# Kernel optimization log

Hardware: AMD Instinct MI355X
Metric: run time of the kernel (lower is better)

Reference implementation:

```python
import jax, jax.numpy as jnp
import numpy as np

BN_EPS = 1e-5
NEG_SLOPE = 0.2


def setup_inputs() -> dict:
    key = jax.random.key(0)
    ks = jax.random.split(key, 3)
    B, C, N, O = 8, 64, 4096, 64
    x = jax.random.normal(ks[0], (B, C, N), dtype=jnp.float32)
    W = jax.random.normal(ks[1], (O, 2 * C), dtype=jnp.float32) * 0.05
    gamma = jnp.ones((O,), dtype=jnp.float32)
    beta = jnp.zeros((O,), dtype=jnp.float32)
    run_mean = jnp.zeros((O,), dtype=jnp.float32)
    run_var = jnp.ones((O,), dtype=jnp.float32)
    return {"x": x, "W": W, "gamma": gamma, "beta": beta,
            "run_mean": run_mean, "run_var": run_var, "k": 20}


def _edgeconv(x, W, gamma, beta, run_mean, run_var, k):
    # x: [B, C, N] -> features [B, N, C]
    xt = jnp.transpose(x, (0, 2, 1))                      # [B, N, C]
    # pairwise_distance = -||xi||^2 + 2 xi.xj - ||xj||^2 (negative sq dist)
    sq = jnp.sum(xt * xt, axis=2, keepdims=True)          # [B, N, 1]
    inner = jnp.einsum('bnc,bmc->bnm', xt, xt)            # [B, N, N]
    pd = 2.0 * inner - sq - jnp.transpose(sq, (0, 2, 1))  # [B, N, N]
    _, idx = jax.lax.top_k(pd, k)                         # [B, N, k] nearest (incl. self)
    # gather neighbor features per batch
    neighbors = jax.vmap(lambda f, i: f[i])(xt, idx)      # [B, N, k, C]
    x_exp = xt[:, :, None, :]                             # [B, N, 1, C]
    edge = jnp.concatenate(
        [jnp.broadcast_to(x_exp, neighbors.shape), neighbors - x_exp], axis=3)  # [B,N,k,2C]
    # 1x1 conv == matmul over channel dim
    y = jnp.einsum('bnkc,oc->bnko', edge, W)              # [B, N, k, O]
    scale = gamma / jnp.sqrt(run_var + BN_EPS)
    y = y * scale + (beta - run_mean * scale)
    y = jnp.where(y >= 0, y, NEG_SLOPE * y)               # LeakyReLU(0.2)
    out = jnp.max(y, axis=2)                              # [B, N, O] max over k
    return jnp.transpose(out, (0, 2, 1))                  # [B, O, N]


def reference(x, W, gamma, beta, run_mean, run_var, k):
    return _edgeconv(x, W, gamma, beta, run_mean, run_var, k)
```

## Files before the change

### kernel.cpp

```cpp
#include <hip/hip_runtime.h>

#define B 8
#define C 64
#define N 4096
#define O 64
#define KNN 20
#define PQ 4
#define BN_EPS 1e-5f
#define NEG_SLOPE 0.2f

typedef _Float16 f16x8 __attribute__((ext_vector_type(8)));
typedef float    f32x4 __attribute__((ext_vector_type(4)));
#define MFMA16(a, b, c) __builtin_amdgcn_mfma_f32_16x16x32_f16(a, b, c, 0, 0, 0)

__device__ __forceinline__ void sorted_insert(float (&d)[KNN], int (&id)[KNN],
                                              float r, int m) {
    bool c[KNN];
    #pragma unroll
    for (int j = 0; j < KNN; ++j) c[j] = d[j] < r;
    #pragma unroll
    for (int j = 0; j < KNN - 1; ++j) {
        d[j]  = __builtin_amdgcn_fmed3f(d[j], d[j + 1], r);
        id[j] = c[j + 1] ? id[j + 1] : (c[j] ? m : id[j]);
    }
    d[KNN - 1]  = c[KNN - 1] ? r : d[KNN - 1];
    id[KNN - 1] = c[KNN - 1] ? m : id[KNN - 1];
}

__global__ __launch_bounds__(256) void k_transpose(const float* __restrict__ x,
                                                   float* __restrict__ Xt,
                                                   float* __restrict__ sq,
                                                   char* __restrict__ AHL) {
    __shared__ float lds[C][65];
    int b    = blockIdx.x >> 6;
    int n0   = (blockIdx.x & 63) << 6;
    int lane = threadIdx.x & 63;
    int w    = threadIdx.x >> 6;
    #pragma unroll
    for (int i = 0; i < 16; ++i) {
        int c = w * 16 + i;
        lds[c][lane] = x[(size_t)b * C * N + (size_t)c * N + n0 + lane];
    }
    __syncthreads();
    #pragma unroll
    for (int i = 0; i < 16; ++i) {
        int nl = w * 16 + i;
        Xt[(size_t)b * N * C + (size_t)(n0 + nl) * C + lane] = lds[lane][nl];
    }
    {
        int n_loc = threadIdx.x >> 2;
        int cg    = threadIdx.x & 3;
        float s = 0.f;
        #pragma unroll
        for (int ii = 0; ii < 16; ++ii) {
            float v = lds[cg * 16 + ii][n_loc];
            s = fmaf(v, v, s);
        }
        s += __shfl_xor(s, 1, 64);
        s += __shfl_xor(s, 2, 64);
        if (cg == 0) sq[b * N + n0 + n_loc] = s;
    }
    int s2  = threadIdx.x & 15;
    int rem = threadIdx.x >> 4;
    int qd  = rem & 3;
    int hh  = (rem >> 2) & 1;
    int tt  = rem >> 3;
    int kb  = hh * 32 + qd * 8;
    for (int i = 0; i < 4; ++i) {
        int rowl = i * 16 + s2;
        f16x8 pk;
        #pragma unroll
        for (int ii = 0; ii < 8; ++ii) {
            float v = lds[kb + ii][rowl];
            _Float16 hv = (_Float16)v;
            if (tt) hv = (_Float16)(v - (float)hv);
            pk[ii] = hv;
        }
        char* dst = AHL + ((size_t)b << 20) + (size_t)((n0 >> 4) + i) * 4096
                  + tt * 2048 + hh * 1024 + qd * 256 + s2 * 16;
        *(f16x8*)dst = pk;
    }
}

__global__ __launch_bounds__(256, 2) void k_ab(const float* __restrict__ Xt,
                                               const float* __restrict__ W,
                                               float* __restrict__ av,
                                               float* __restrict__ bv) {
    int b  = blockIdx.x & 7;
    int n0 = ((blockIdx.x >> 3) & 31) << 7;
    int o  = threadIdx.x & 63;
    int w  = __builtin_amdgcn_readfirstlane((int)(threadIdx.x >> 6));
    float wa[C], wb[C];
    #pragma unroll
    for (int c = 0; c < C; ++c) {
        float w1 = W[o * 2 * C + c];
        float w2 = W[o * 2 * C + C + c];
        wa[c] = w1 - w2;
        wb[c] = w2;
    }
    const float* xb = Xt + (size_t)b * N * C;
    for (int i = 0; i < 32; ++i) {
        int n = n0 + w * 32 + i;
        const float4* xr4 = (const float4*)(xb + (size_t)n * C);
        float aa = 0.f, bb = 0.f;
        #pragma unroll
        for (int c4 = 0; c4 < C / 4; ++c4) {
            float4 xv = xr4[c4];
            aa = fmaf(xv.x, wa[c4 * 4 + 0], aa);
            bb = fmaf(xv.x, wb[c4 * 4 + 0], bb);
            aa = fmaf(xv.y, wa[c4 * 4 + 1], aa);
            bb = fmaf(xv.y, wb[c4 * 4 + 1], bb);
            aa = fmaf(xv.z, wa[c4 * 4 + 2], aa);
            bb = fmaf(xv.z, wb[c4 * 4 + 2], bb);
            aa = fmaf(xv.w, wa[c4 * 4 + 3], aa);
            bb = fmaf(xv.w, wb[c4 * 4 + 3], bb);
        }
        size_t oidx = ((size_t)b * N + n) * O + o;
        av[oidx] = aa;
        bv[oidx] = bb;
    }
}

__global__ __launch_bounds__(64, 2) void k_knn(const char* __restrict__ AHL,
                                               const float* __restrict__ sq,
                                               float* __restrict__ pdg,
                                               int* __restrict__ pig) {
    int bid  = blockIdx.x;
    int qg   = bid >> 4;
    int b    = bid & 7;
    int h    = (bid >> 3) & 1;
    int lane = threadIdx.x & 63;
    int quad = lane >> 4;
    const char*  AHLb = AHL + ((size_t)b << 20);
    const float* sqb  = sq + b * N;
    int cbase0 = h * (N / 2);
    const char* Asrc = AHLb + (size_t)cbase0 * 256;

    const char* qb = AHLb + (size_t)qg * 4096 + lane * 16;
    f16x8 bh0 = *(const f16x8*)(qb);
    f16x8 bh1 = *(const f16x8*)(qb + 1024);
    f16x8 bl0 = *(const f16x8*)(qb + 2048);
    f16x8 bl1 = *(const f16x8*)(qb + 3072);

    float d[KNN]; int id[KNN];
    float pv[PQ]; int pi[PQ]; int pc = 0;
    #pragma unroll
    for (int j = 0; j < PQ; ++j) { pv[j] = 0.f; pi[j] = 0; }

    const char* p0 = Asrc + lane * 16;
    f16x8 na0 = *(const f16x8*)(p0);
    f16x8 na1 = *(const f16x8*)(p0 + 1024);
    f16x8 na2 = *(const f16x8*)(p0 + 2048);
    f16x8 na3 = *(const f16x8*)(p0 + 3072);
    float4 nsq = *(const float4*)(sqb + cbase0 + quad * 4);

    #pragma unroll
    for (int it = 0; it < 5; ++it) {
        f16x8 a0 = na0, a1 = na1, a2 = na2, a3 = na3;
        float4 sqv = nsq;
        {
            const char* p = Asrc + (size_t)(it + 1) * 4096 + lane * 16;
            na0 = *(const f16x8*)(p);
            na1 = *(const f16x8*)(p + 1024);
            na2 = *(const f16x8*)(p + 2048);
            na3 = *(const f16x8*)(p + 3072);
            nsq = *(const float4*)(sqb + cbase0 + (it + 1) * 16 + quad * 4);
        }
        f32x4 acc = {0.f, 0.f, 0.f, 0.f};
        acc = MFMA16(a0, bh0, acc);
        acc = MFMA16(a1, bh1, acc);
        acc = MFMA16(a0, bl0, acc);
        acc = MFMA16(a1, bl1, acc);
        acc = MFMA16(a2, bh0, acc);
        acc = MFMA16(a3, bh1, acc);
        int c0 = cbase0 + it * 16 + quad * 4;
        #pragma unroll
        for (int r = 0; r < 4; ++r) {
            float sc = fmaf(2.f, acc[r],
                            -((r == 0) ? sqv.x : (r == 1) ? sqv.y
                                       : (r == 2) ? sqv.z : sqv.w));
            d[it * 4 + r]  = sc;
            id[it * 4 + r] = c0 + r;
        }
    }
    #pragma unroll
    for (int i = 0; i < KNN - 1; ++i) {
        #pragma unroll
        for (int j = 0; j < KNN - 1 - i; ++j) {
            bool sw = d[j] > d[j + 1];
            float tv = d[j]; int ti = id[j];
            d[j]      = sw ? d[j + 1] : d[j];
            id[j]     = sw ? id[j + 1] : id[j];
            d[j + 1]  = sw ? tv : d[j + 1];
            id[j + 1] = sw ? ti : id[j + 1];
        }
    }
    float thr = d[0];
    thr = fmaxf(thr, __shfl_xor(thr, 16, 64));
    thr = fmaxf(thr, __shfl_xor(thr, 32, 64));

    #pragma unroll 1
    for (int it = 5; it < 128; ++it) {
        f16x8 a0 = na0, a1 = na1, a2 = na2, a3 = na3;
        float4 sqv = nsq;
        if (it + 1 < 128) {
            const char* p = Asrc + (size_t)(it + 1) * 4096 + lane * 16;
            na0 = *(const f16x8*)(p);
            na1 = *(const f16x8*)(p + 1024);
            na2 = *(const f16x8*)(p + 2048);
            na3 = *(const f16x8*)(p + 3072);
            nsq = *(const float4*)(sqb + cbase0 + (it + 1) * 16 + quad * 4);
        }
        f32x4 acc = {0.f, 0.f, 0.f, 0.f};
        acc = MFMA16(a0, bh0, acc);
        acc = MFMA16(a1, bh1, acc);
        acc = MFMA16(a0, bl0, acc);
        acc = MFMA16(a1, bl1, acc);
        acc = MFMA16(a2, bh0, acc);
        acc = MFMA16(a3, bh1, acc);
        int c0 = cbase0 + it * 16 + quad * 4;
        #pragma unroll
        for (int r = 0; r < 4; ++r) {
            float sc = fmaf(2.f, acc[r],
                            -((r == 0) ? sqv.x : (r == 1) ? sqv.y
                                       : (r == 2) ? sqv.z : sqv.w));
            if (sc > thr) {
                #pragma unroll
                for (int j = 0; j < PQ; ++j) {
                    bool sel = (pc == j);
                    pv[j] = sel ? sc : pv[j];
                    pi[j] = sel ? (c0 + r) : pi[j];
                }
                ++pc;
            }
            if (__any(pc == PQ)) {
                #pragma unroll
                for (int j = 0; j < PQ; ++j)
                    if (j < pc && pv[j] > d[0]) sorted_insert(d, id, pv[j], pi[j]);
                pc = 0;
                float t = d[0];
                t = fmaxf(t, __shfl_xor(t, 16, 64));
                t = fmaxf(t, __shfl_xor(t, 32, 64));
                thr = fmaxf(thr, t);
            }
        }
    }
    #pragma unroll
    for (int j = 0; j < PQ; ++j)
        if (j < pc && pv[j] > d[0]) sorted_insert(d, id, pv[j], pi[j]);

    #pragma unroll 1
    for (int step = 0; step < 2; ++step) {
        int off = (step == 0) ? 32 : 16;
        bool active = (step == 0) ? (quad < 2) : (quad == 0);
        for (int j = KNN - 1; j >= 0; --j) {
            float rv = __shfl(d[j], lane + off, 64);
            int   ri = __shfl(id[j], lane + off, 64);
            bool ins = active && (rv > d[0]);
            if (!__any(ins)) break;
            if (ins) sorted_insert(d, id, rv, ri);
        }
    }
    if (lane < 16) {
        size_t rr = (size_t)b * N + qg * 16 + lane;
        float* po = pdg + (rr * 2 + h) * KNN;
        int*   qo = pig + (rr * 2 + h) * KNN;
        #pragma unroll
        for (int j = 0; j < KNN; ++j) { po[j] = d[j]; qo[j] = id[j]; }
    }
}

__global__ __launch_bounds__(128) void k_merge(const float* __restrict__ pdg,
                                               const int* __restrict__ pig,
                                               int* __restrict__ knn) {
    __shared__ float sd[128][41];
    __shared__ int   si[128][41];
    int t = threadIdx.x;
    size_t rr = (size_t)blockIdx.x * 128 + t;
    const float* pr = pdg + rr * (2 * KNN);
    const int*   qr = pig + rr * (2 * KNN);
    #pragma unroll
    for (int j = 0; j < 2 * KNN; ++j) { sd[t][j] = pr[j]; si[t][j] = qr[j]; }
    int i = KNN - 1, j = KNN - 1;
    int* op = knn + rr * KNN;
    for (int o = 0; o < KNN; ++o) {
        bool t0 = (j < 0) || (i >= 0 && sd[t][i] >= sd[t][KNN + j]);
        op[o] = t0 ? si[t][i] : si[t][KNN + j];
        if (t0) --i; else --j;
    }
}

__global__ __launch_bounds__(256) void k_out(const float* __restrict__ av,
                                             const float* __restrict__ bv,
                                             const int* __restrict__ knn,
                                             const float* __restrict__ gamma,
                                             const float* __restrict__ beta,
                                             const float* __restrict__ rmean,
                                             const float* __restrict__ rvar,
                                             float* __restrict__ out) {
    __shared__ float lds[64][65];
    int b    = blockIdx.x & 7;
    int n0   = (blockIdx.x >> 3) << 6;
    int lane = threadIdx.x & 63;
    int w    = __builtin_amdgcn_readfirstlane((int)(threadIdx.x >> 6));
    int o    = lane;
    float scale = gamma[o] * rsqrtf(rvar[o] + BN_EPS);
    float bias  = fmaf(-rmean[o], scale, beta[o]);
    const float* bvb = bv + (size_t)b * N * O;
    for (int i = 0; i < 16; ++i) {
        int n = n0 + w * 16 + i;
        const int* kn = knn + ((size_t)b * N + n) * KNN;
        float mx = -3.4e38f, mn = 3.4e38f;
        #pragma unroll
        for (int j = 0; j < KNN; ++j) {
            float v = bvb[(size_t)kn[j] * O + o];
            mx = fmaxf(mx, v);
            mn = fminf(mn, v);
        }
        float a   = av[((size_t)b * N + n) * O + o];
        float sel = (scale >= 0.f) ? (a + mx) : (a + mn);
        float y   = fmaf(sel, scale, bias);
        y = fmaxf(y, NEG_SLOPE * y);
        lds[o][w * 16 + i] = y;
    }
    __syncthreads();
    int r  = threadIdx.x >> 2;
    int c0 = (threadIdx.x & 3) << 4;
    float* ob = out + (size_t)b * O * N + (size_t)r * N + n0;
    #pragma unroll
    for (int j = 0; j < 16; j += 4) {
        float4 v;
        v.x = lds[r][c0 + j + 0];
        v.y = lds[r][c0 + j + 1];
        v.z = lds[r][c0 + j + 2];
        v.w = lds[r][c0 + j + 3];
        *(float4*)(ob + c0 + j) = v;
    }
}

extern "C" void kernel_launch(void* const* d_in, const int* in_sizes, int n_in,
                              void* d_out, int out_size, void* d_ws, size_t ws_size,
                              hipStream_t stream) {
    const float* x     = (const float*)d_in[0];
    const float* W     = (const float*)d_in[1];
    const float* gamma = (const float*)d_in[2];
    const float* beta  = (const float*)d_in[3];
    const float* rmean = (const float*)d_in[4];
    const float* rvar  = (const float*)d_in[5];
    float* out = (float*)d_out;

    char* wsb = (char*)d_ws;
    float* Xt  = (float*)(wsb);
    float* sqn = (float*)(wsb + 8388608);
    float* av  = (float*)(wsb + 8519680);
    float* bvv = (float*)(wsb + 16908288);
    int*   knn = (int*)  (wsb + 25296896);
    char*  AHL =         (wsb + 27918336);
    float* pdg = (float*)(wsb + 36306944);
    int*   pig = (int*)  (wsb + 41549824);

    k_transpose<<<512, 256, 0, stream>>>(x, Xt, sqn, AHL);
    k_ab<<<256, 256, 0, stream>>>(Xt, W, av, bvv);
    k_knn<<<4096, 64, 0, stream>>>(AHL, sqn, pdg, pig);
    k_merge<<<256, 128, 0, stream>>>(pdg, pig, knn);
    k_out<<<512, 256, 0, stream>>>(av, bvv, knn, gamma, beta, rmean, rvar, out);
}
```

Baseline: 371.3 us.

## Split KNN candidate range into quarters with two waves per block

Each k_knn block now runs two wavefronts, and each wave scans a quarter of the candidate points instead of a half. This doubles the parallel wave count and halves each wave's serial loop. The merge kernel now combines four partial top-k lists through two pairwise merges, and partial indices are stored as 16-bit values in workspace reused from the transpose buffer. The cost is more partial-list traffic and more merge work, plus less per-wave filtering warmup, since each wave's threshold starts from fewer candidates.

Measured after the change: 411.1 us. 1.11x slower.

```diff
diff --git a/kernel.cpp b/kernel.cpp
--- a/kernel.cpp
+++ b/kernel.cpp
@@ -121,19 +121,21 @@
     }
 }
 
-__global__ __launch_bounds__(64, 2) void k_knn(const char* __restrict__ AHL,
-                                               const float* __restrict__ sq,
-                                               float* __restrict__ pdg,
-                                               int* __restrict__ pig) {
+__global__ __launch_bounds__(128, 2) void k_knn(const char* __restrict__ AHL,
+                                                const float* __restrict__ sq,
+                                                float* __restrict__ pdg,
+                                                unsigned short* __restrict__ pig) {
     int bid  = blockIdx.x;
     int qg   = bid >> 4;
     int b    = bid & 7;
-    int h    = (bid >> 3) & 1;
+    int qh   = (bid >> 3) & 1;
+    int w    = __builtin_amdgcn_readfirstlane((int)(threadIdx.x >> 6));
+    int q    = qh * 2 + w;
     int lane = threadIdx.x & 63;
     int quad = lane >> 4;
     const char*  AHLb = AHL + ((size_t)b << 20);
     const float* sqb  = sq + b * N;
-    int cbase0 = h * (N / 2);
+    int cbase0 = q * (N / 4);
     const char* Asrc = AHLb + (size_t)cbase0 * 256;
 
     const char* qb = AHLb + (size_t)qg * 4096 + lane * 16;
@@ -200,10 +202,10 @@
     thr = fmaxf(thr, __shfl_xor(thr, 32, 64));
 
     #pragma unroll 1
-    for (int it = 5; it < 128; ++it) {
+    for (int it = 5; it < 64; ++it) {
         f16x8 a0 = na0, a1 = na1, a2 = na2, a3 = na3;
         float4 sqv = nsq;
-        if (it + 1 < 128) {
+        if (it + 1 < 64) {
             const char* p = Asrc + (size_t)(it + 1) * 4096 + lane * 16;
             na0 = *(const f16x8*)(p);
             na1 = *(const f16x8*)(p + 1024);
@@ -263,30 +265,48 @@
     }
     if (lane < 16) {
         size_t rr = (size_t)b * N + qg * 16 + lane;
-        float* po = pdg + (rr * 2 + h) * KNN;
-        int*   qo = pig + (rr * 2 + h) * KNN;
-        #pragma unroll
-        for (int j = 0; j < KNN; ++j) { po[j] = d[j]; qo[j] = id[j]; }
-    }
-}
-
-__global__ __launch_bounds__(128) void k_merge(const float* __restrict__ pdg,
-                                               const int* __restrict__ pig,
-                                               int* __restrict__ knn) {
-    __shared__ float sd[128][41];
-    __shared__ int   si[128][41];
+        float*          po = pdg + (rr * 4 + q) * KNN;
+        unsigned short* qo = pig + (rr * 4 + q) * KNN;
+        #pragma unroll
+        for (int j = 0; j < KNN; ++j) {
+            po[j] = d[j];
+            qo[j] = (unsigned short)id[j];
+        }
+    }
+}
+
+__global__ __launch_bounds__(64) void k_merge(const float* __restrict__ pdg,
+                                              const unsigned short* __restrict__ pig,
+                                              int* __restrict__ knn) {
+    __shared__ float sd[64][121];
+    __shared__ int   si[64][121];
     int t = threadIdx.x;
-    size_t rr = (size_t)blockIdx.x * 128 + t;
-    const float* pr = pdg + rr * (2 * KNN);
-    const int*   qr = pig + rr * (2 * KNN);
-    #pragma unroll
-    for (int j = 0; j < 2 * KNN; ++j) { sd[t][j] = pr[j]; si[t][j] = qr[j]; }
+    size_t rr = (size_t)blockIdx.x * 64 + t;
+    const float*          pr = pdg + rr * (4 * KNN);
+    const unsigned short* qr = pig + rr * (4 * KNN);
+    #pragma unroll
+    for (int j = 0; j < 4 * KNN; ++j) { sd[t][j] = pr[j]; si[t][j] = qr[j]; }
+    #pragma unroll
+    for (int pair = 0; pair < 2; ++pair) {
+        int a0 = pair * 2 * KNN;
+        int b0 = a0 + KNN;
+        int o0 = 4 * KNN + pair * KNN;
+        int i = KNN - 1, j = KNN - 1;
+        #pragma unroll 1
+        for (int k = KNN - 1; k >= 0; --k) {
+            bool ta = (j < 0) || (i >= 0 && sd[t][a0 + i] >= sd[t][b0 + j]);
+            sd[t][o0 + k] = ta ? sd[t][a0 + i] : sd[t][b0 + j];
+            si[t][o0 + k] = ta ? si[t][a0 + i] : si[t][b0 + j];
+            if (ta) --i; else --j;
+        }
+    }
     int i = KNN - 1, j = KNN - 1;
     int* op = knn + rr * KNN;
+    #pragma unroll 1
     for (int o = 0; o < KNN; ++o) {
-        bool t0 = (j < 0) || (i >= 0 && sd[t][i] >= sd[t][KNN + j]);
-        op[o] = t0 ? si[t][i] : si[t][KNN + j];
-        if (t0) --i; else --j;
+        bool ta = (j < 0) || (i >= 0 && sd[t][4 * KNN + i] >= sd[t][5 * KNN + j]);
+        op[o] = ta ? si[t][4 * KNN + i] : si[t][5 * KNN + j];
+        if (ta) --i; else --j;
     }
 }
 
@@ -351,17 +371,17 @@
 
     char* wsb = (char*)d_ws;
     float* Xt  = (float*)(wsb);
+    unsigned short* pig = (unsigned short*)(wsb);
     float* sqn = (float*)(wsb + 8388608);
     float* av  = (float*)(wsb + 8519680);
     float* bvv = (float*)(wsb + 16908288);
     int*   knn = (int*)  (wsb + 25296896);
     char*  AHL =         (wsb + 27918336);
     float* pdg = (float*)(wsb + 36306944);
-    int*   pig = (int*)  (wsb + 41549824);
 
     k_transpose<<<512, 256, 0, stream>>>(x, Xt, sqn, AHL);
     k_ab<<<256, 256, 0, stream>>>(Xt, W, av, bvv);
-    k_knn<<<4096, 64, 0, stream>>>(AHL, sqn, pdg, pig);
-    k_merge<<<256, 128, 0, stream>>>(pdg, pig, knn);
+    k_knn<<<4096, 128, 0, stream>>>(AHL, sqn, pdg, pig);
+    k_merge<<<512, 64, 0, stream>>>(pdg, pig, knn);
     k_out<<<512, 256, 0, stream>>>(av, bvv, knn, gamma, beta, rmean, rvar, out);
 }
```
